# Optimization experiments

Hardware: AMD Instinct MI355X
Metric: run time of the kernel (lower is better)

Reference implementation:

```python
import jax, jax.numpy as jnp
import numpy as np

PAD, SOS, EOS = 0, 1, 2
NEG = -10000.0


def _lstm(x, w_ih, w_hh, b, reverse):
    # x: [T,B,E]; torch gate order i,f,g,o; b = b_ih + b_hh combined
    T, B, _ = x.shape
    H = w_hh.shape[1]
    xg = jnp.einsum('tbe,ge->tbg', x, w_ih) + b  # precompute input gates [T,B,4H]

    def step(carry, g):
        h, c = carry
        g = g + h @ w_hh.T
        i, f, gg, o = jnp.split(g, 4, axis=-1)
        c = jax.nn.sigmoid(f) * c + jax.nn.sigmoid(i) * jnp.tanh(gg)
        h = jax.nn.sigmoid(o) * jnp.tanh(c)
        return (h, c), h

    init = (jnp.zeros((B, H), x.dtype), jnp.zeros((B, H), x.dtype))
    _, hs = jax.lax.scan(step, init, xg, reverse=reverse)
    return hs  # [T,B,H]


def setup_inputs() -> dict:
    key = jax.random.key(0)
    T, B, V, E, H, K = 256, 64, 50000, 512, 512, 24
    ks = jax.random.split(key, 12)
    xw = jax.random.randint(ks[0], (T, B), 4, V)
    y_tags = jax.random.randint(ks[1], (T, B), 3, K)  # real tags, > EOS so mask is all ones
    y0 = jnp.concatenate([jnp.full((1, B), SOS, dtype=y_tags.dtype), y_tags], axis=0)  # [T+1,B]
    s = lambda k, sh: (jax.random.normal(k, sh, jnp.float32) * 0.02)
    emb = s(ks[2], (V, E))
    w_ih_f = s(ks[3], (4 * H, E)); w_hh_f = s(ks[4], (4 * H, H)); b_f = jnp.zeros((4 * H,), jnp.float32)
    w_ih_b = s(ks[5], (4 * H, E)); w_hh_b = s(ks[6], (4 * H, H)); b_b = jnp.zeros((4 * H,), jnp.float32)
    w_out = s(ks[7], (K, 2 * H)); b_out = jnp.zeros((K,), jnp.float32)
    trans = jax.random.normal(ks[8], (K, K), jnp.float32)
    trans = trans.at[SOS, :].set(NEG).at[:, EOS].set(NEG).at[:, PAD].set(NEG).at[PAD, :].set(NEG)
    trans = trans.at[PAD, EOS].set(0.0).at[PAD, PAD].set(0.0)
    return dict(xw=xw, y0=y0, emb=emb, w_ih_f=w_ih_f, w_hh_f=w_hh_f, b_f=b_f,
                w_ih_b=w_ih_b, w_hh_b=w_hh_b, b_b=b_b, w_out=w_out, b_out=b_out, trans=trans)


def reference(xw, y0, emb, w_ih_f, w_hh_f, b_f, w_ih_b, w_hh_b, b_b, w_out, b_out, trans):
    mask = (y0[1:] > PAD).astype(emb.dtype)  # [T,B]
    x = emb[xw]  # [T,B,E]
    hf = _lstm(x, w_ih_f, w_hh_f, b_f, reverse=False)
    hb = _lstm(x, w_ih_b, w_hh_b, b_b, reverse=True)
    h = jnp.concatenate([hf, hb], axis=-1) @ w_out.T + b_out  # [T,B,K]
    h = h * mask[:, :, None]
    B, K = h.shape[1], h.shape[2]

    # --- CRF partition function (forward algorithm) ---
    score0 = jnp.full((B, K), NEG, h.dtype).at[:, SOS].set(0.0)

    def step(score, inp):
        ht, mt = inp  # ht: [B,K], mt: [B]
        # new[b,j] = logsumexp_i(score[b,i] + ht[b,j] + trans[j,i])
        new = jax.nn.logsumexp(score[:, None, :] + ht[:, :, None] + trans[None, :, :], axis=2)
        return new * mt[:, None] + score * (1.0 - mt[:, None]), None

    score, _ = jax.lax.scan(step, score0, (h, mask))
    Z = jax.nn.logsumexp(score + trans[EOS], axis=1)  # [B]

    # --- gold path score ---
    emit = jnp.take_along_axis(h, y0[1:][:, :, None], axis=2)[..., 0]  # [T,B]
    tr = trans[y0[1:], y0[:-1]]  # [T,B]
    lens = mask.sum(0).astype(jnp.int32)  # [B]
    last = jnp.take_along_axis(y0, lens[None, :], axis=0)[0]  # y0[lens[b], b]
    gold = ((emit + tr) * mask).sum(0) + trans[EOS, last]  # [B]

    return jnp.mean(Z - gold)
```

## Files before the change

### kernel.cpp

```cpp
#include <hip/hip_runtime.h>

typedef __attribute__((ext_vector_type(8))) short short8;
typedef __attribute__((ext_vector_type(4))) float f32x4;

#define NEGV -10000.0f

__device__ __forceinline__ float bfu2f(unsigned short u) {
  unsigned int x = ((unsigned int)u) << 16;
  return __builtin_bit_cast(float, x);
}
__device__ __forceinline__ unsigned short f2bfu(float f) {
  unsigned int x = __builtin_bit_cast(unsigned int, f);
  x += 0x7fffu + ((x >> 16) & 1u);
  return (unsigned short)(x >> 16);
}
__device__ __forceinline__ float fsig(float x) {
  return 1.0f / (1.0f + __expf(-x));
}
__device__ __forceinline__ float ftanh(float x) {
  x = fminf(15.0f, fmaxf(-15.0f, x));
  float e = __expf(-2.0f * x);
  return (1.0f - e) / (1.0f + e);
}

__global__ __launch_bounds__(256) void prep_kernel(
    const float* __restrict__ wihf, const float* __restrict__ wihb,
    const float* __restrict__ whhf, const float* __restrict__ whhb,
    const float* __restrict__ wo, const float* __restrict__ bfv,
    const float* __restrict__ bbv,
    unsigned short* __restrict__ wih_c, unsigned short* __restrict__ whh_c,
    unsigned short* __restrict__ wout_c, float* __restrict__ bias_c) {
  size_t i = (size_t)blockIdx.x * 256 + threadIdx.x;
  const size_t n_half = 2048u * 512u;
  const size_t n_wih = 2u * n_half;
  const size_t n_wo = 24u * 1024u;
  if (i < n_wih) {
    float v = (i < n_half) ? wihf[i] : wihb[i - n_half];
    wih_c[i] = f2bfu(v);
  } else if (i < 2u * n_wih) {
    size_t j = i - n_wih;
    float v = (j < n_half) ? whhf[j] : whhb[j - n_half];
    whh_c[j] = f2bfu(v);
  } else if (i < 2u * n_wih + n_wo) {
    size_t j = i - 2u * n_wih;
    wout_c[j] = f2bfu(wo[j]);
  } else if (i < 2u * n_wih + n_wo + 4096u) {
    size_t j = i - 2u * n_wih - n_wo;
    bias_c[j] = (j < 2048u) ? bfv[j] : bbv[j - 2048u];
  }
}

__global__ __launch_bounds__(64) void gather_kernel(
    const int* __restrict__ xw, const float* __restrict__ emb,
    unsigned short* __restrict__ xbf) {
  int tb = blockIdx.x;
  int l = threadIdx.x;
  int tok = xw[tb];
  const float* src = emb + (size_t)tok * 512 + l * 8;
  short8 o;
#pragma unroll
  for (int j = 0; j < 8; ++j) o[j] = (short)f2bfu(src[j]);
  *(short8*)(xbf + (size_t)tb * 512 + l * 8) = o;
}

__global__ __launch_bounds__(256) void gemm_xg_kernel(
    const unsigned short* __restrict__ A,
    const unsigned short* __restrict__ Bm,
    const float* __restrict__ bias,
    unsigned short* __restrict__ C) {
  __shared__ alignas(16) char As[16384];
  __shared__ alignas(16) char Bs[16384];
  int m0 = blockIdx.x * 128, n0 = blockIdx.y * 128;
  int tid = threadIdx.x;
  int wv = tid >> 6, l = tid & 63;
  int wm = wv >> 1, wn = wv & 1;
  int col = l & 15, quad = l >> 4;
  f32x4 zero4 = {0.f, 0.f, 0.f, 0.f};
  f32x4 acc[4][4];
#pragma unroll
  for (int i = 0; i < 4; ++i)
#pragma unroll
    for (int j = 0; j < 4; ++j) acc[i][j] = zero4;
  for (int kt = 0; kt < 8; ++kt) {
#pragma unroll
    for (int q = 0; q < 4; ++q) {
      int o = q * 4096 + tid * 16;
      int row = o >> 7;
      int cb = o & 127;
      int swz = cb ^ ((row & 7) << 4);
      short8 va = *(const short8*)(A + (size_t)(m0 + row) * 512 + kt * 64 + (cb >> 1));
      *(short8*)(As + row * 128 + swz) = va;
      short8 vb = *(const short8*)(Bm + (size_t)(n0 + row) * 512 + kt * 64 + (cb >> 1));
      *(short8*)(Bs + row * 128 + swz) = vb;
    }
    __syncthreads();
#pragma unroll
    for (int kk = 0; kk < 2; ++kk) {
      short8 af[4], bf8[4];
#pragma unroll
      for (int mi = 0; mi < 4; ++mi) {
        int r = wm * 64 + mi * 16 + col;
        int cb = kk * 64 + quad * 16;
        af[mi] = *(const short8*)(As + r * 128 + (cb ^ ((r & 7) << 4)));
      }
#pragma unroll
      for (int ni = 0; ni < 4; ++ni) {
        int r = wn * 64 + ni * 16 + col;
        int cb = kk * 64 + quad * 16;
        bf8[ni] = *(const short8*)(Bs + r * 128 + (cb ^ ((r & 7) << 4)));
      }
#pragma unroll
      for (int mi = 0; mi < 4; ++mi)
#pragma unroll
        for (int ni = 0; ni < 4; ++ni)
          acc[mi][ni] = __builtin_amdgcn_mfma_f32_16x16x32_bf16(af[mi], bf8[ni], acc[mi][ni], 0, 0, 0);
    }
    __syncthreads();
  }
#pragma unroll
  for (int ni = 0; ni < 4; ++ni) {
    int cg = n0 + wn * 64 + ni * 16 + col;
    float bv = bias[cg];
#pragma unroll
    for (int mi = 0; mi < 4; ++mi) {
#pragma unroll
      for (int r = 0; r < 4; ++r) {
        int rg = m0 + wm * 64 + mi * 16 + quad * 4 + r;
        C[(size_t)rg * 4096 + cg] = f2bfu(acc[mi][ni][r] + bv);
      }
    }
  }
}

__global__ __launch_bounds__(64, 1) void scan_kernel(
    const unsigned short* __restrict__ whh,
    const unsigned short* __restrict__ xg,
    unsigned short* __restrict__ hfp,
    unsigned short* __restrict__ hbp) {
  __shared__ alignas(16) unsigned short tbuf[128];
  int wid = blockIdx.x;
  int l = threadIdx.x;
  int c = wid & 7;
  int dir = c & 1;
  int wv = (c >> 1) & 3;
  int g = wid >> 3;
  int u0 = g * 8;
  int col = l & 15, quad = l >> 4;
  int b_row = wv * 16 + quad * 4;
  short8 bfr[2][16];
#pragma unroll
  for (int n = 0; n < 2; ++n) {
    int blk = n * 2 + (col >> 3);
    int gr = blk * 512 + u0 + (col & 7);
    const char* base = (const char*)(whh + ((size_t)dir * 2048 + gr) * 512 + quad * 8);
#pragma unroll
    for (int kk = 0; kk < 16; ++kk)
      asm volatile("global_load_dwordx4 %0, %1, off" : "=v"(bfr[n][kk]) : "v"(base + kk * 64));
  }
  unsigned short* hseq = dir ? hbp : hfp;
  int gc0 = dir * 2048 + (col >> 3) * 512 + u0 + (col & 7);
  float cst[4] = {0.f, 0.f, 0.f, 0.f};
  f32x4 zero4 = {0.f, 0.f, 0.f, 0.f};
  short8 af[16];
  int usefast = 1;
  unsigned int xA[8], xB[8];
  {
    int t0 = dir ? 255 : 0;
#pragma unroll
    for (int r = 0; r < 4; ++r) {
      const char* xa = (const char*)(xg + ((size_t)t0 * 64 + b_row + r) * 4096 + gc0);
      asm volatile("global_load_ushort %0, %1, off" : "=v"(xA[r]) : "v"(xa));
      asm volatile("global_load_ushort %0, %1, off" : "=v"(xA[4 + r]) : "v"(xa + 2048));
    }
  }
  asm volatile("s_waitcnt vmcnt(0)" ::: "memory");
  __builtin_amdgcn_sched_barrier(0);

#define SCAN_STEP(S_, XU_, XP_)                                                             \
  {                                                                                         \
    int s_ = (S_);                                                                          \
    int t_ = dir ? (255 - s_) : s_;                                                         \
    f32x4 a0 = zero4, a1 = zero4;                                                           \
    if (s_ > 0) {                                                                           \
      int tprev = t_ + (dir ? 1 : -1);                                                      \
      const char* pbase = (const char*)hseq + (size_t)tprev * 65536 + quad * 1024 +         \
                          (wv * 16 + col) * 16;                                             \
      unsigned long long bal = 1ull;                                                        \
      if (usefast) {                                                                        \
        for (int tryi = 0; tryi < 8 && bal != 0ull; ++tryi) {                               \
          _Pragma("unroll") for (int kk = 0; kk < 16; ++kk)                                 \
              asm volatile("global_load_dwordx4 %0, %1, off sc0"                            \
                           : "=v"(af[kk]) : "v"(pbase + kk * 4096));                        \
          asm volatile("s_waitcnt vmcnt(0)" ::: "memory");                                  \
          __builtin_amdgcn_sched_barrier(0);                                                \
          unsigned int st_ = 0u;                                                            \
          _Pragma("unroll") for (int kk = 0; kk < 16; ++kk)                                 \
              st_ |= (((unsigned short)af[kk][0]) == 0xFFFFu) ? 1u : 0u;                    \
          bal = __ballot(st_ != 0u);                                                        \
        }                                                                                   \
        if (bal != 0ull) usefast = 0;                                                       \
      }                                                                                     \
      while (bal != 0ull) {                                                                 \
        _Pragma("unroll") for (int kk = 0; kk < 16; ++kk)                                   \
            asm volatile("global_load_dwordx4 %0, %1, off sc0 sc1"                          \
                         : "=v"(af[kk]) : "v"(pbase + kk * 4096));                          \
        asm volatile("s_waitcnt vmcnt(0)" ::: "memory");                                    \
        __builtin_amdgcn_sched_barrier(0);                                                  \
        unsigned int st_ = 0u;                                                              \
        _Pragma("unroll") for (int kk = 0; kk < 16; ++kk)                                   \
            st_ |= (((unsigned short)af[kk][0]) == 0xFFFFu) ? 1u : 0u;                      \
        bal = __ballot(st_ != 0u);                                                          \
      }                                                                                     \
      __builtin_amdgcn_s_setprio(1);                                                        \
      __builtin_amdgcn_sched_barrier(0);                                                    \
      _Pragma("unroll") for (int kk = 0; kk < 16; ++kk) {                                   \
        a0 = __builtin_amdgcn_mfma_f32_16x16x32_bf16(af[kk], bfr[0][kk], a0, 0, 0, 0);      \
        a1 = __builtin_amdgcn_mfma_f32_16x16x32_bf16(af[kk], bfr[1][kk], a1, 0, 0, 0);      \
      }                                                                                     \
    }                                                                                       \
    {                                                                                       \
      int sn = (s_ < 255) ? (s_ + 1) : 255;                                                 \
      int tn = dir ? (255 - sn) : sn;                                                       \
      _Pragma("unroll") for (int r = 0; r < 4; ++r) {                                       \
        const char* xa = (const char*)(xg + ((size_t)tn * 64 + b_row + r) * 4096 + gc0);    \
        asm volatile("global_load_ushort %0, %1, off" : "=v"(XP_[r]) : "v"(xa));            \
        asm volatile("global_load_ushort %0, %1, off" : "=v"(XP_[4 + r]) : "v"(xa + 2048)); \
      }                                                                                     \
    }                                                                                       \
    {                                                                                       \
      bool low = (col < 8);                                                                 \
      _Pragma("unroll") for (int r = 0; r < 4; ++r) {                                       \
        float g0 = a0[r] + bfu2f((unsigned short)XU_[r]);                                   \
        float g1 = a1[r] + bfu2f((unsigned short)XU_[4 + r]);                               \
        float p0 = __shfl_xor(g0, 8);                                                       \
        float p1 = __shfl_xor(g1, 8);                                                       \
        float iv = low ? g0 : p0;                                                           \
        float fv = low ? p0 : g0;                                                           \
        float gv = low ? g1 : p1;                                                           \
        float ov = low ? p1 : g1;                                                           \
        float cn = fsig(fv) * cst[r] + fsig(iv) * ftanh(gv);                                \
        cst[r] = cn;                                                                        \
        float hv = fsig(ov) * ftanh(cn);                                                    \
        if (low) tbuf[(quad * 4 + r) * 8 + (col & 7)] = f2bfu(hv);                          \
      }                                                                                     \
    }                                                                                       \
    asm volatile("s_waitcnt lgkmcnt(0)" ::: "memory");                                      \
    if (l < 16) {                                                                           \
      short8 hrow = *(const short8*)(tbuf + l * 8);                                         \
      char* dst = (char*)hseq + (size_t)t_ * 65536 + g * 1024 + (wv * 16 + l) * 16;         \
      asm volatile("global_store_dwordx4 %0, %1, off sc0 sc1" ::"v"(dst), "v"(hrow)         \
                   : "memory");                                                             \
      asm volatile("global_store_dwordx4 %0, %1, off sc0" ::"v"(dst), "v"(hrow)             \
                   : "memory");                                                             \
    }                                                                                       \
    __builtin_amdgcn_s_setprio(0);                                                          \
  }

  for (int it = 0; it < 128; ++it) {
    SCAN_STEP(2 * it, xA, xB);
    SCAN_STEP(2 * it + 1, xB, xA);
  }
#undef SCAN_STEP
}

__global__ __launch_bounds__(256) void logits_kernel(
    const unsigned short* __restrict__ hfp, const unsigned short* __restrict__ hbp,
    const unsigned short* __restrict__ wout, const float* __restrict__ bout,
    const int* __restrict__ y0, float* __restrict__ lg) {
  int t = blockIdx.x, tid = threadIdx.x;
  int b = tid >> 2, ks = tid & 3;
  int ytag = y0[(t + 1) * 64 + b];
  float mk = (ytag > 0) ? 1.f : 0.f;
  float av[6] = {0.f, 0.f, 0.f, 0.f, 0.f, 0.f};
  const char* pf = (const char*)hfp + (size_t)t * 65536;
  const char* pb = (const char*)hbp + (size_t)t * 65536;
  for (int uc = 0; uc < 64; ++uc) {
    short8 hv = *(const short8*)(pf + uc * 1024 + b * 16);
#pragma unroll
    for (int kk = 0; kk < 6; ++kk) {
      int k = ks * 6 + kk;
      short8 wv = *(const short8*)(wout + (size_t)k * 1024 + uc * 8);
#pragma unroll
      for (int j = 0; j < 8; ++j)
        av[kk] += bfu2f((unsigned short)hv[j]) * bfu2f((unsigned short)wv[j]);
    }
  }
  for (int uc = 0; uc < 64; ++uc) {
    short8 hv = *(const short8*)(pb + uc * 1024 + b * 16);
#pragma unroll
    for (int kk = 0; kk < 6; ++kk) {
      int k = ks * 6 + kk;
      short8 wv = *(const short8*)(wout + (size_t)k * 1024 + 512 + uc * 8);
#pragma unroll
      for (int j = 0; j < 8; ++j)
        av[kk] += bfu2f((unsigned short)hv[j]) * bfu2f((unsigned short)wv[j]);
    }
  }
#pragma unroll
  for (int kk = 0; kk < 6; ++kk) {
    int k = ks * 6 + kk;
    lg[((size_t)t * 64 + b) * 32 + k] = mk * (av[kk] + bout[k]);
  }
}

__global__ __launch_bounds__(64) void crf_kernel(
    const float* __restrict__ lg, const int* __restrict__ y0,
    const float* __restrict__ trans, float* __restrict__ res) {
  int b = blockIdx.x, l = threadIdx.x;
  __shared__ float tl[600];
  __shared__ float sc[24];
  for (int i = l; i < 576; i += 64) tl[(i / 24) * 25 + (i % 24)] = trans[i];
  if (l < 24) sc[l] = (l == 1) ? 0.f : NEGV;
  __syncthreads();
  float gold = 0.f;
  int lens = 0;
  for (int t = l; t < 256; t += 64) {
    int y1 = y0[(t + 1) * 64 + b];
    int yp = y0[t * 64 + b];
    if (y1 > 0) {
      gold += lg[((size_t)t * 64 + b) * 32 + y1] + tl[y1 * 25 + yp];
      lens += 1;
    }
  }
#pragma unroll
  for (int off = 32; off > 0; off >>= 1) {
    gold += __shfl_down(gold, off);
    lens += __shfl_down(lens, off);
  }
  gold = __shfl(gold, 0);
  lens = __shfl(lens, 0);
  int last = y0[lens * 64 + b];
  gold += tl[2 * 25 + last];
  int lc = (l < 24) ? l : 23;
  float trow[24];
#pragma unroll
  for (int j = 0; j < 24; ++j) trow[j] = tl[lc * 25 + j];
  for (int t = 0; t < 256; ++t) {
    int y1 = y0[(t + 1) * 64 + b];
    if (y1 > 0) {
      float ns = 0.f;
      if (l < 24) {
        float ht = lg[((size_t)t * 64 + b) * 32 + l];
        float mx = -3.0e38f;
        float sj[24];
#pragma unroll
        for (int j = 0; j < 24; ++j) {
          sj[j] = sc[j] + trow[j];
          mx = fmaxf(mx, sj[j]);
        }
        float sm = 0.f;
#pragma unroll
        for (int j = 0; j < 24; ++j) sm += __expf(sj[j] - mx);
        ns = ht + mx + __logf(sm);
      }
      __syncthreads();
      if (l < 24) sc[l] = ns;
      __syncthreads();
    }
  }
  float v = (l < 24) ? sc[l] + tl[2 * 25 + l] : -3.0e38f;
  float mx = v;
#pragma unroll
  for (int off = 32; off > 0; off >>= 1) mx = fmaxf(mx, __shfl_xor(mx, off));
  float se = (l < 24) ? __expf(v - mx) : 0.f;
#pragma unroll
  for (int off = 32; off > 0; off >>= 1) se += __shfl_xor(se, off);
  float Z = mx + __logf(se);
  if (l == 0) res[b] = Z - gold;
}

__global__ __launch_bounds__(64) void reduce_kernel(const float* __restrict__ res,
                                                    float* __restrict__ out) {
  int l = threadIdx.x;
  float v = res[l];
#pragma unroll
  for (int off = 32; off > 0; off >>= 1) v += __shfl_down(v, off);
  if (l == 0) out[0] = v * (1.0f / 64.0f);
}

extern "C" void kernel_launch(void* const* d_in, const int* in_sizes, int n_in,
                              void* d_out, int out_size, void* d_ws, size_t ws_size,
                              hipStream_t stream) {
  (void)in_sizes; (void)n_in; (void)out_size; (void)ws_size;
  const int* xw = (const int*)d_in[0];
  const int* y0 = (const int*)d_in[1];
  const float* emb = (const float*)d_in[2];
  const float* wihf = (const float*)d_in[3];
  const float* whhf = (const float*)d_in[4];
  const float* bfv = (const float*)d_in[5];
  const float* wihb = (const float*)d_in[6];
  const float* whhb = (const float*)d_in[7];
  const float* bbv = (const float*)d_in[8];
  const float* wo = (const float*)d_in[9];
  const float* bo = (const float*)d_in[10];
  const float* tr = (const float*)d_in[11];
  char* ws = (char*)d_ws;
  unsigned short* xg = (unsigned short*)(ws + 0);
  unsigned short* xbf = (unsigned short*)(ws + 134217728);
  unsigned short* wih_c = (unsigned short*)(ws + 150994944);
  unsigned short* whh_c = (unsigned short*)(ws + 155189248);
  unsigned short* wout_c = (unsigned short*)(ws + 159383552);
  float* bias_c = (float*)(ws + 159432704);
  unsigned short* hfp = (unsigned short*)(ws + 159449088);
  unsigned short* hbp = (unsigned short*)(ws + 176226304);
  float* lg = (float*)(ws + 193003520);
  float* res = (float*)(ws + 195104768);

  hipMemsetAsync(hfp, 0xFF, 16777216, stream);
  hipMemsetAsync(hbp, 0xFF, 16777216, stream);
  prep_kernel<<<16496, 256, 0, stream>>>(wihf, wihb, whhf, whhb, wo, bfv, bbv,
                                         wih_c, whh_c, wout_c, bias_c);
  gather_kernel<<<16384, 64, 0, stream>>>(xw, emb, xbf);
  gemm_xg_kernel<<<dim3(128, 32), 256, 0, stream>>>(xbf, wih_c, bias_c, xg);
  scan_kernel<<<512, 64, 0, stream>>>(whh_c, xg, hfp, hbp);
  logits_kernel<<<256, 256, 0, stream>>>(hfp, hbp, wout_c, bo, y0, lg);
  crf_kernel<<<64, 64, 0, stream>>>(lg, y0, tr, res);
  reduce_kernel<<<1, 64, 0, stream>>>(res, (float*)d_out);
}
```

Before: 1.208 ms.

## Fuse embedding gather into input GEMM and simplify scan polling and stores

Drops the separate gather kernel: the input-gate GEMM now reads fp32 embedding rows directly by token index and converts them to bf16 while staging tiles into shared memory. This saves one launch and a round trip through an intermediate buffer, but every one of the 32 N-tile blocks re-reads and re-converts the same fp32 rows. In the scan kernel, block-to-work mapping is remapped, the two-phase polling loop becomes a single coherent do-while, MFMA accumulation is split into even/odd chains to break dependency latency, and the duplicate hidden-state store is removed.

```diff
diff --git a/kernel.cpp b/kernel.cpp
--- a/kernel.cpp
+++ b/kernel.cpp
@@ -50,21 +50,9 @@
   }
 }
 
-__global__ __launch_bounds__(64) void gather_kernel(
-    const int* __restrict__ xw, const float* __restrict__ emb,
-    unsigned short* __restrict__ xbf) {
-  int tb = blockIdx.x;
-  int l = threadIdx.x;
-  int tok = xw[tb];
-  const float* src = emb + (size_t)tok * 512 + l * 8;
-  short8 o;
-#pragma unroll
-  for (int j = 0; j < 8; ++j) o[j] = (short)f2bfu(src[j]);
-  *(short8*)(xbf + (size_t)tb * 512 + l * 8) = o;
-}
-
 __global__ __launch_bounds__(256) void gemm_xg_kernel(
-    const unsigned short* __restrict__ A,
+    const int* __restrict__ xw,
+    const float* __restrict__ emb,
     const unsigned short* __restrict__ Bm,
     const float* __restrict__ bias,
     unsigned short* __restrict__ C) {
@@ -75,6 +63,9 @@
   int wv = tid >> 6, l = tid & 63;
   int wm = wv >> 1, wn = wv & 1;
   int col = l & 15, quad = l >> 4;
+  int tok[4];
+#pragma unroll
+  for (int q = 0; q < 4; ++q) tok[q] = xw[m0 + ((q * 4096 + tid * 16) >> 7)];
   f32x4 zero4 = {0.f, 0.f, 0.f, 0.f};
   f32x4 acc[4][4];
 #pragma unroll
@@ -88,7 +79,15 @@
       int row = o >> 7;
       int cb = o & 127;
       int swz = cb ^ ((row & 7) << 4);
-      short8 va = *(const short8*)(A + (size_t)(m0 + row) * 512 + kt * 64 + (cb >> 1));
+      const float* sa = emb + (size_t)tok[q] * 512 + kt * 64 + (cb >> 1);
+      f32x4 f0 = *(const f32x4*)sa;
+      f32x4 f1 = *(const f32x4*)(sa + 4);
+      short8 va;
+#pragma unroll
+      for (int j = 0; j < 4; ++j) {
+        va[j] = (short)f2bfu(f0[j]);
+        va[4 + j] = (short)f2bfu(f1[j]);
+      }
       *(short8*)(As + row * 128 + swz) = va;
       short8 vb = *(const short8*)(Bm + (size_t)(n0 + row) * 512 + kt * 64 + (cb >> 1));
       *(short8*)(Bs + row * 128 + swz) = vb;
@@ -140,10 +139,9 @@
   __shared__ alignas(16) unsigned short tbuf[128];
   int wid = blockIdx.x;
   int l = threadIdx.x;
-  int c = wid & 7;
-  int dir = c & 1;
-  int wv = (c >> 1) & 3;
-  int g = wid >> 3;
+  int dir = wid & 1;
+  int g = (wid >> 1) & 63;
+  int wv = (wid >> 7) & 3;
   int u0 = g * 8;
   int col = l & 15, quad = l >> 4;
   int b_row = wv * 16 + quad * 4;
@@ -162,7 +160,6 @@
   float cst[4] = {0.f, 0.f, 0.f, 0.f};
   f32x4 zero4 = {0.f, 0.f, 0.f, 0.f};
   short8 af[16];
-  int usefast = 1;
   unsigned int xA[8], xB[8];
   {
     int t0 = dir ? 255 : 0;
@@ -180,27 +177,13 @@
   {                                                                                         \
     int s_ = (S_);                                                                          \
     int t_ = dir ? (255 - s_) : s_;                                                         \
-    f32x4 a0 = zero4, a1 = zero4;                                                           \
+    f32x4 ae0 = zero4, ao0 = zero4, ae1 = zero4, ao1 = zero4;                               \
     if (s_ > 0) {                                                                           \
       int tprev = t_ + (dir ? 1 : -1);                                                      \
       const char* pbase = (const char*)hseq + (size_t)tprev * 65536 + quad * 1024 +         \
                           (wv * 16 + col) * 16;                                             \
-      unsigned long long bal = 1ull;                                                        \
-      if (usefast) {                                                                        \
-        for (int tryi = 0; tryi < 8 && bal != 0ull; ++tryi) {                               \
-          _Pragma("unroll") for (int kk = 0; kk < 16; ++kk)                                 \
-              asm volatile("global_load_dwordx4 %0, %1, off sc0"                            \
-                           : "=v"(af[kk]) : "v"(pbase + kk * 4096));                        \
-          asm volatile("s_waitcnt vmcnt(0)" ::: "memory");                                  \
-          __builtin_amdgcn_sched_barrier(0);                                                \
-          unsigned int st_ = 0u;                                                            \
-          _Pragma("unroll") for (int kk = 0; kk < 16; ++kk)                                 \
-              st_ |= (((unsigned short)af[kk][0]) == 0xFFFFu) ? 1u : 0u;                    \
-          bal = __ballot(st_ != 0u);                                                        \
-        }                                                                                   \
-        if (bal != 0ull) usefast = 0;                                                       \
-      }                                                                                     \
-      while (bal != 0ull) {                                                                 \
+      unsigned long long bal;                                                               \
+      do {                                                                                  \
         _Pragma("unroll") for (int kk = 0; kk < 16; ++kk)                                   \
             asm volatile("global_load_dwordx4 %0, %1, off sc0 sc1"                          \
                          : "=v"(af[kk]) : "v"(pbase + kk * 4096));                          \
@@ -210,12 +193,18 @@
         _Pragma("unroll") for (int kk = 0; kk < 16; ++kk)                                   \
             st_ |= (((unsigned short)af[kk][0]) == 0xFFFFu) ? 1u : 0u;                      \
         bal = __ballot(st_ != 0u);                                                          \
-      }                                                                                     \
+      } while (bal != 0ull);                                                                \
       __builtin_amdgcn_s_setprio(1);                                                        \
       __builtin_amdgcn_sched_barrier(0);                                                    \
-      _Pragma("unroll") for (int kk = 0; kk < 16; ++kk) {                                   \
-        a0 = __builtin_amdgcn_mfma_f32_16x16x32_bf16(af[kk], bfr[0][kk], a0, 0, 0, 0);      \
-        a1 = __builtin_amdgcn_mfma_f32_16x16x32_bf16(af[kk], bfr[1][kk], a1, 0, 0, 0);      \
+      _Pragma("unroll") for (int kk = 0; kk < 8; ++kk) {                                    \
+        ae0 = __builtin_amdgcn_mfma_f32_16x16x32_bf16(af[2 * kk], bfr[0][2 * kk], ae0, 0,   \
+                                                      0, 0);                                \
+        ae1 = __builtin_amdgcn_mfma_f32_16x16x32_bf16(af[2 * kk], bfr[1][2 * kk], ae1, 0,   \
+                                                      0, 0);                                \
+        ao0 = __builtin_amdgcn_mfma_f32_16x16x32_bf16(af[2 * kk + 1], bfr[0][2 * kk + 1],   \
+                                                      ao0, 0, 0, 0);                        \
+        ao1 = __builtin_amdgcn_mfma_f32_16x16x32_bf16(af[2 * kk + 1], bfr[1][2 * kk + 1],   \
+                                                      ao1, 0, 0, 0);                        \
       }                                                                                     \
     }                                                                                       \
     {                                                                                       \
@@ -230,8 +219,8 @@
     {                                                                                       \
       bool low = (col < 8);                                                                 \
       _Pragma("unroll") for (int r = 0; r < 4; ++r) {                                       \
-        float g0 = a0[r] + bfu2f((unsigned short)XU_[r]);                                   \
-        float g1 = a1[r] + bfu2f((unsigned short)XU_[4 + r]);                               \
+        float g0 = ae0[r] + ao0[r] + bfu2f((unsigned short)XU_[r]);                         \
+        float g1 = ae1[r] + ao1[r] + bfu2f((unsigned short)XU_[4 + r]);                     \
         float p0 = __shfl_xor(g0, 8);                                                       \
         float p1 = __shfl_xor(g1, 8);                                                       \
         float iv = low ? g0 : p0;                                                           \
@@ -250,8 +239,6 @@
       char* dst = (char*)hseq + (size_t)t_ * 65536 + g * 1024 + (wv * 16 + l) * 16;         \
       asm volatile("global_store_dwordx4 %0, %1, off sc0 sc1" ::"v"(dst), "v"(hrow)         \
                    : "memory");                                                             \
-      asm volatile("global_store_dwordx4 %0, %1, off sc0" ::"v"(dst), "v"(hrow)             \
-                   : "memory");                                                             \
     }                                                                                       \
     __builtin_amdgcn_s_setprio(0);                                                          \
   }
@@ -396,7 +383,6 @@
   const float* tr = (const float*)d_in[11];
   char* ws = (char*)d_ws;
   unsigned short* xg = (unsigned short*)(ws + 0);
-  unsigned short* xbf = (unsigned short*)(ws + 134217728);
   unsigned short* wih_c = (unsigned short*)(ws + 150994944);
   unsigned short* whh_c = (unsigned short*)(ws + 155189248);
   unsigned short* wout_c = (unsigned short*)(ws + 159383552);
@@ -410,8 +396,7 @@
   hipMemsetAsync(hbp, 0xFF, 16777216, stream);
   prep_kernel<<<16496, 256, 0, stream>>>(wihf, wihb, whhf, whhb, wo, bfv, bbv,
                                          wih_c, whh_c, wout_c, bias_c);
-  gather_kernel<<<16384, 64, 0, stream>>>(xw, emb, xbf);
-  gemm_xg_kernel<<<dim3(128, 32), 256, 0, stream>>>(xbf, wih_c, bias_c, xg);
+  gemm_xg_kernel<<<dim3(128, 32), 256, 0, stream>>>(xw, emb, wih_c, bias_c, xg);
   scan_kernel<<<512, 64, 0, stream>>>(whh_c, xg, hfp, hbp);
   logits_kernel<<<256, 256, 0, stream>>>(hfp, hbp, wout_c, bo, y0, lg);
   crf_kernel<<<64, 64, 0, stream>>>(lg, y0, tr, res);
```

Result: slower. 1.316 ms (+8.9%).
